# Optimization experiments

Measured on AMD Instinct MI355X. Metric: run time of the kernel, lower is better.

Reference implementation:

```python
import jax, jax.numpy as jnp
import numpy as np

B, T, D, H = 4, 1024, 512, 8
DK = D // H
P = 2 * T - 1  # relative position length


def rel_shift(x):
    # x: (b, h, t, 2t-1) -> (b, h, t, t), Transformer-XL relative shift
    b, h, t, p = x.shape
    x = jnp.pad(x, ((0, 0), (0, 0), (0, 0), (1, 0)))  # (b,h,t,p+1)
    x = x.reshape(b, h, p + 1, t)[:, :, 1:, :].reshape(b, h, t, p)
    return x[..., :t]


def setup_inputs() -> dict:
    key = jax.random.key(0)
    ks = jax.random.split(key, 16)
    s = 0.02
    return {
        "q": jax.random.normal(ks[0], (B, T, D), jnp.float32),
        "k": jax.random.normal(ks[1], (B, T, D), jnp.float32),
        "v": jax.random.normal(ks[2], (B, T, D), jnp.float32),
        "pos_emb": jax.random.normal(ks[3], (1, P, D), jnp.float32),
        "Wq": jax.random.normal(ks[4], (D, D), jnp.float32) * s,
        "bq": jnp.zeros((D,), jnp.float32),
        "Wk": jax.random.normal(ks[5], (D, D), jnp.float32) * s,
        "bk": jnp.zeros((D,), jnp.float32),
        "Wv": jax.random.normal(ks[6], (D, D), jnp.float32) * s,
        "bv": jnp.zeros((D,), jnp.float32),
        "Wp": jax.random.normal(ks[7], (D, D), jnp.float32) * s,
        "pos_bias_u": jax.random.normal(ks[8], (H, DK), jnp.float32) * s,
        "pos_bias_v": jax.random.normal(ks[9], (H, DK), jnp.float32) * s,
        "Wo": jax.random.normal(ks[10], (D, D), jnp.float32) * s,
        "bo": jnp.zeros((D,), jnp.float32),
    }


def reference(q, k, v, pos_emb, Wq, bq, Wk, bk, Wv, bv, Wp,
              pos_bias_u, pos_bias_v, Wo, bo):
    b, t, d = q.shape
    # QKV projections, split heads -> (b, t, h, dk)
    qh = (q @ Wq.T + bq).reshape(b, t, H, DK)
    kh = (k @ Wk.T + bk).reshape(b, t, H, DK)
    vh = (v @ Wv.T + bv).reshape(b, t, H, DK)
    # positional projection (no bias): (1, P, h, dk)
    ph = (pos_emb @ Wp.T).reshape(pos_emb.shape[1], H, DK)
    # content term: (q + u) . k
    q_u = qh + pos_bias_u  # (b,t,h,dk)
    matrix_ac = jnp.einsum("bqhd,bkhd->bhqk", q_u, kh)
    # position term: (q + v) . p, then relative shift
    q_v = qh + pos_bias_v
    matrix_bd = jnp.einsum("bqhd,phd->bhqp", q_v, ph)
    matrix_bd = rel_shift(matrix_bd)  # (b,h,t,t)
    scores = (matrix_ac + matrix_bd) / jnp.sqrt(jnp.float32(DK))
    attn = jax.nn.softmax(scores, axis=-1)
    out = jnp.einsum("bhqk,bkhd->bqhd", attn, vh).reshape(b, t, d)
    return out @ Wo.T + bo
```

## Files before the change

### kernel.cpp

```cpp
#include <hip/hip_runtime.h>
#include <math.h>

typedef unsigned short u16;
typedef _Float16 f16;
typedef __attribute__((ext_vector_type(8))) _Float16 f16x8;
typedef __attribute__((ext_vector_type(4))) float f32x4;

#define B_  4
#define T_  1024
#define D_  512
#define H_  8
#define DK_ 64
#define P_  2047

#define MFMAH(a, b, c) __builtin_amdgcn_mfma_f32_16x16x32_f16(a, b, c, 0, 0, 0)

__device__ __forceinline__ u16 f2hbits(float x) {
    union { f16 h; u16 u; } cv; cv.h = (f16)x; return cv.u;
}

__device__ __forceinline__ void gload_lds16(const u16* g, u16* l) {
    __builtin_amdgcn_global_load_lds(
        (const __attribute__((address_space(1))) void*)g,
        (__attribute__((address_space(3))) void*)l, 16, 0, 0);
}

__device__ __forceinline__ int swz8(int row, int colbase) {
    return row * 64 + (((colbase >> 3) ^ (row & 7)) << 3);
}

__global__ __launch_bounds__(256)
void conv_all(const float* __restrict__ q, const float* __restrict__ k,
              const float* __restrict__ v, const float* __restrict__ pe,
              const float* __restrict__ wq, const float* __restrict__ wk,
              const float* __restrict__ wv, const float* __restrict__ wp,
              const float* __restrict__ wo,
              u16* qs, u16* ks, u16* vs, u16* pes,
              u16* wqs, u16* wks, u16* wvs, u16* wps, u16* wos)
{
    const int NQ = 524288;
    const int NPE = 262016;
    const int NW = 65536;
    const int TOT = 3 * NQ + NPE + 5 * NW;
    for (int i = blockIdx.x * 256 + threadIdx.x; i < TOT; i += gridDim.x * 256) {
        const float* src; u16* dst; int off;
        int j = i;
        if (j < NQ)              { src = q;  dst = qs;  off = j; }
        else if ((j -= NQ) < NQ) { src = k;  dst = ks;  off = j; }
        else if ((j -= NQ) < NQ) { src = v;  dst = vs;  off = j; }
        else if ((j -= NQ) < NPE){ src = pe; dst = pes; off = j; }
        else if ((j -= NPE) < NW){ src = wq; dst = wqs; off = j; }
        else if ((j -= NW) < NW) { src = wk; dst = wks; off = j; }
        else if ((j -= NW) < NW) { src = wv; dst = wvs; off = j; }
        else if ((j -= NW) < NW) { src = wp; dst = wps; off = j; }
        else                     { j -= NW; src = wo; dst = wos; off = j; }
        float4 x = *(const float4*)(src + (size_t)off * 4);
        union { f16 h[4]; uint2 u2; } cv;
        cv.h[0] = (f16)x.x; cv.h[1] = (f16)x.y;
        cv.h[2] = (f16)x.z; cv.h[3] = (f16)x.w;
        *(uint2*)(dst + (size_t)off * 4) = cv.u2;
    }
}

__device__ __forceinline__ void gemm_core(
    const u16* __restrict__ A, const u16* __restrict__ Bw,
    int bm, int bn, int M, f32x4 (&acc)[4][4],
    u16 (&sA)[128][64], u16 (&sB)[128][64])
{
    const int tid = threadIdx.x;
    const int ln = tid & 63, w = tid >> 6;
    const int arow = ln & 15, kseg = ln >> 4;
    const int wr = w >> 1, wc = w & 1;

    for (int k0 = 0; k0 < 512; k0 += 64) {
        #pragma unroll
        for (int it = 0; it < 4; ++it) {
            int ch = it * 256 + tid;
            int r = ch >> 3, j = ch & 7;
            int rm = bm + r; if (rm > M - 1) rm = M - 1;
            gload_lds16(A + (size_t)rm * 512 + k0 + ((j ^ (r & 7)) << 3),
                        &sA[0][0] + ch * 8);
        }
        #pragma unroll
        for (int it = 0; it < 4; ++it) {
            int ch = it * 256 + tid;
            int r = ch >> 3, j = ch & 7;
            gload_lds16(Bw + (size_t)(bn + r) * 512 + k0 + ((j ^ (r & 7)) << 3),
                        &sB[0][0] + ch * 8);
        }
        __syncthreads();

        f16x8 af[4][2], bf[4][2];
        #pragma unroll
        for (int mi = 0; mi < 4; ++mi) {
            int row = wr * 64 + mi * 16 + arow;
            #pragma unroll
            for (int kc = 0; kc < 2; ++kc)
                af[mi][kc] = *(const f16x8*)
                    (&sA[row][0] + ((((kc << 2) | kseg) ^ (row & 7)) << 3));
        }
        #pragma unroll
        for (int nj = 0; nj < 4; ++nj) {
            int row = wc * 64 + nj * 16 + arow;
            #pragma unroll
            for (int kc = 0; kc < 2; ++kc)
                bf[nj][kc] = *(const f16x8*)
                    (&sB[row][0] + ((((kc << 2) | kseg) ^ (row & 7)) << 3));
        }
        #pragma unroll
        for (int mi = 0; mi < 4; ++mi)
            #pragma unroll
            for (int nj = 0; nj < 4; ++nj)
                #pragma unroll
                for (int kc = 0; kc < 2; ++kc)
                    acc[mi][nj] = MFMAH(af[mi][kc], bf[nj][kc], acc[mi][nj]);
        __syncthreads();
    }
}

__global__ __launch_bounds__(256, 3)
void gemm_qkvp(const u16* __restrict__ qs, const u16* __restrict__ ks,
               const u16* __restrict__ vs, const u16* __restrict__ pes,
               const u16* __restrict__ wqs, const u16* __restrict__ wks,
               const u16* __restrict__ wvs, const u16* __restrict__ wps,
               const float* __restrict__ bq, const float* __restrict__ bk,
               const float* __restrict__ bv,
               float* __restrict__ qh, u16* __restrict__ kh,
               u16* __restrict__ vt, u16* __restrict__ ph)
{
    __shared__ u16 sA[128][64];
    __shared__ u16 sB[128][64];

    const int by = blockIdx.y;
    const u16 *A, *Bw; const float* bias;
    int seg, bm, M, Tn;
    if (by < 32)      { seg=0; bm=by*128;       A=qs;  Bw=wqs; bias=bq;      M=4096; Tn=T_; }
    else if (by < 64) { seg=1; bm=(by-32)*128;  A=ks;  Bw=wks; bias=bk;      M=4096; Tn=T_; }
    else if (by < 96) { seg=2; bm=(by-64)*128;  A=vs;  Bw=wvs; bias=bv;      M=4096; Tn=T_; }
    else              { seg=3; bm=(by-96)*128;  A=pes; Bw=wps; bias=nullptr; M=P_;   Tn=P_; }
    const int bn = blockIdx.x * 128;

    f32x4 acc[4][4] = {};
    gemm_core(A, Bw, bm, bn, M, acc, sA, sB);

    const int tid = threadIdx.x;
    const int ln = tid & 63, w = tid >> 6;
    const int arow = ln & 15, kseg = ln >> 4;
    const int wr = w >> 1, wc = w & 1;

    float bv0[4];
    #pragma unroll
    for (int nj = 0; nj < 4; ++nj)
        bv0[nj] = bias ? bias[bn + wc * 64 + nj * 16 + arow] : 0.f;

    #pragma unroll
    for (int mi = 0; mi < 4; ++mi)
        #pragma unroll
        for (int r = 0; r < 4; ++r) {
            int m = bm + wr * 64 + mi * 16 + kseg * 4 + r;
            if (m >= M) continue;
            #pragma unroll
            for (int nj = 0; nj < 4; ++nj) {
                int n = bn + wc * 64 + nj * 16 + arow;
                float val = acc[mi][nj][r] + bv0[nj];
                if (seg == 0) {
                    qh[(size_t)m * 512 + n] = val;
                } else if (seg == 2) {
                    int bb = m >> 10, t = m & 1023;
                    int hh = n >> 6, d = n & 63;
                    vt[((size_t)(bb * H_ + hh) * 64 + d) * T_ + t] = f2hbits(val);
                } else {
                    int bb = (Tn == T_) ? (m >> 10) : 0;
                    int t = m - bb * Tn;
                    int hh = n >> 6, d = n & 63;
                    size_t off = ((size_t)(bb * H_ + hh) * Tn + t) * 64 + d;
                    if (seg == 1) kh[off] = f2hbits(val);
                    else          ph[off] = f2hbits(val);
                }
            }
        }
}

__global__ __launch_bounds__(256, 3)
void gemm_out(const u16* __restrict__ A, const u16* __restrict__ Bw,
              const float* __restrict__ bias, float* __restrict__ C)
{
    __shared__ u16 sA[128][64];
    __shared__ u16 sB[128][64];
    const int bn = blockIdx.x * 128;
    const int bm = blockIdx.y * 128;
    f32x4 acc[4][4] = {};
    gemm_core(A, Bw, bm, bn, 4096, acc, sA, sB);

    const int tid = threadIdx.x;
    const int ln = tid & 63, w = tid >> 6;
    const int arow = ln & 15, kseg = ln >> 4;
    const int wr = w >> 1, wc = w & 1;
    #pragma unroll
    for (int mi = 0; mi < 4; ++mi)
        #pragma unroll
        for (int r = 0; r < 4; ++r) {
            int m = bm + wr * 64 + mi * 16 + kseg * 4 + r;
            #pragma unroll
            for (int nj = 0; nj < 4; ++nj) {
                int n = bn + wc * 64 + nj * 16 + arow;
                C[(size_t)m * 512 + n] = acc[mi][nj][r] + bias[n];
            }
        }
}

__global__ __launch_bounds__(256, 2)
void relattn_mfma(const float* __restrict__ qh,
                  const u16* __restrict__ kh, const u16* __restrict__ vt,
                  const u16* __restrict__ ph,
                  const float* __restrict__ pbu, const float* __restrict__ pbv,
                  u16* __restrict__ ao)
{
    __shared__ u16 s_k[2][64][64];
    __shared__ u16 s_p[2][64][64];
    __shared__ u16 s_pp[4][16][64];

    const int tid = threadIdx.x;
    const int ln  = tid & 63;
    const int w   = tid >> 6;
    const int arow = ln & 15;
    const int kseg = ln >> 4;

    const int lg = ((blockIdx.x & 7) << 6) | (blockIdx.x >> 3);
    const int qt = lg & 15, h = (lg >> 4) & 7, b = lg >> 7;
    const int q0 = qt * 64;

    f16x8 qu[2], qv[2];
    #pragma unroll
    for (int c = 0; c < 2; ++c) {
        const float* qp = qh + ((size_t)(b * T_ + q0 + w * 16 + arow)) * D_ + h * DK_ + c * 32 + kseg * 8;
        float4 a0 = *(const float4*)qp;
        float4 a1 = *(const float4*)(qp + 4);
        const float* up = pbu + h * DK_ + c * 32 + kseg * 8;
        const float* vp = pbv + h * DK_ + c * 32 + kseg * 8;
        float4 u0 = *(const float4*)up, u1 = *(const float4*)(up + 4);
        float4 v0 = *(const float4*)vp, v1 = *(const float4*)(vp + 4);
        float qa[8] = {a0.x, a0.y, a0.z, a0.w, a1.x, a1.y, a1.z, a1.w};
        float ua[8] = {u0.x, u0.y, u0.z, u0.w, u1.x, u1.y, u1.z, u1.w};
        float va[8] = {v0.x, v0.y, v0.z, v0.w, v1.x, v1.y, v1.z, v1.w};
        #pragma unroll
        for (int i = 0; i < 8; ++i) {
            qu[c][i] = (f16)((qa[i] + ua[i]) * 0.125f);
            qv[c][i] = (f16)((qa[i] + va[i]) * 0.125f);
        }
    }

    f32x4 o_[4] = {};
    float m_run[4] = {-1e30f, -1e30f, -1e30f, -1e30f};
    float l_run[4] = {};

    const size_t kvbase = (size_t)(b * H_ + h) * T_ * 64;
    const size_t vtbase = (size_t)(b * H_ + h) * 64 * T_;
    const size_t pbase  = (size_t)h * P_ * 64;
    const int jb0 = 960 - q0;

    auto stage_k = [&](int kt, int buf) {
        #pragma unroll
        for (int it = 0; it < 2; ++it) {
            int idx = tid + it * 256;
            int r = idx >> 3, ch = idx & 7;
            const u16* src = kh + kvbase + (size_t)(kt * 64 + r) * 64 + ((ch ^ (r & 7)) << 3);
            gload_lds16(src, &s_k[buf][0][0] + idx * 8);
        }
    };
    auto stage_p = [&](int c, int slot) {
        #pragma unroll
        for (int it = 0; it < 2; ++it) {
            int idx = tid + it * 256;
            int r = idx >> 3, ch = idx & 7;
            int j = jb0 + c * 64 + r; if (j > P_ - 1) j = P_ - 1;
            const u16* src = ph + pbase + (size_t)j * 64 + ((ch ^ (r & 7)) << 3);
            gload_lds16(src, &s_p[slot][0][0] + idx * 8);
        }
    };
    auto bd_chunk = [&](int slot, f32x4* out) {
        #pragma unroll
        for (int nb = 0; nb < 4; ++nb) {
            int pr = nb * 16 + arow;
            f16x8 b0 = *(const f16x8*)(&s_p[slot][0][0] + swz8(pr, kseg * 8));
            f16x8 b1 = *(const f16x8*)(&s_p[slot][0][0] + swz8(pr, 32 + kseg * 8));
            out[nb] = MFMAH(qv[0], b0, out[nb]);
            out[nb] = MFMAH(qv[1], b1, out[nb]);
        }
    };

    stage_k(0, 0); stage_p(0, 0); stage_p(1, 1);
    __syncthreads();
    f32x4 carry[4] = {};
    bd_chunk(0, carry);
    __syncthreads();

    for (int t = 0; t < 16; ++t) {
        const int p = t & 1;
        const int k0 = t * 64;

        if (t < 15) { stage_k(t + 1, p ^ 1); stage_p(t + 2, p); }

        f16x8 vfr[4][2];
        #pragma unroll
        for (int nt = 0; nt < 4; ++nt) {
            const u16* vp = vt + vtbase + (size_t)(nt * 16 + arow) * T_ + k0 + kseg * 8;
            vfr[nt][0] = *(const f16x8*)vp;
            vfr[nt][1] = *(const f16x8*)(vp + 32);
        }

        __builtin_amdgcn_s_setprio(1);
        f32x4 ac[4] = {};
        #pragma unroll
        for (int nt = 0; nt < 4; ++nt) {
            int kr = nt * 16 + arow;
            f16x8 b0 = *(const f16x8*)(&s_k[p][0][0] + swz8(kr, kseg * 8));
            f16x8 b1 = *(const f16x8*)(&s_k[p][0][0] + swz8(kr, 32 + kseg * 8));
            ac[nt] = MFMAH(qu[0], b0, ac[nt]);
            ac[nt] = MFMAH(qu[1], b1, ac[nt]);
        }
        f32x4 bdn[4] = {};
        bd_chunk(p ^ 1, bdn);
        __builtin_amdgcn_s_setprio(0);

        float win[5][4];
        #pragma unroll
        for (int r = 0; r < 4; ++r) {
            if (w == 0)      { win[0][r]=carry[3][r]; win[1][r]=bdn[0][r];   win[2][r]=bdn[1][r];   win[3][r]=bdn[2][r];   win[4][r]=bdn[3][r]; }
            else if (w == 1) { win[0][r]=carry[2][r]; win[1][r]=carry[3][r]; win[2][r]=bdn[0][r];   win[3][r]=bdn[1][r];   win[4][r]=bdn[2][r]; }
            else if (w == 2) { win[0][r]=carry[1][r]; win[1][r]=carry[2][r]; win[2][r]=carry[3][r]; win[3][r]=bdn[0][r];   win[4][r]=bdn[1][r]; }
            else             { win[0][r]=carry[0][r]; win[1][r]=carry[1][r]; win[2][r]=carry[2][r]; win[3][r]=carry[3][r]; win[4][r]=bdn[0][r]; }
        }

        float sm[4][4];
        #pragma unroll
        for (int r = 0; r < 4; ++r) {
            int sl  = 15 - (kseg << 2) - r;
            int src = (ln & 48) | ((arow + sl) & 15);
            int cy  = (arow + sl) >> 4;
            float pm[5];
            #pragma unroll
            for (int i = 0; i < 5; ++i) pm[i] = __shfl(win[i][r], src, 64);
            #pragma unroll
            for (int nt = 0; nt < 4; ++nt)
                sm[nt][r] = ac[nt][r] + (cy ? pm[nt + 1] : pm[nt]);
        }

        #pragma unroll
        for (int r = 0; r < 4; ++r) {
            float mxv = fmaxf(fmaxf(sm[0][r], sm[1][r]), fmaxf(sm[2][r], sm[3][r]));
            #pragma unroll
            for (int off = 8; off; off >>= 1) mxv = fmaxf(mxv, __shfl_xor(mxv, off));
            float mnew = fmaxf(m_run[r], mxv);
            float fac = __expf(m_run[r] - mnew);
            m_run[r] = mnew;
            float ps = 0.f;
            int r16 = kseg * 4 + r;
            #pragma unroll
            for (int nt = 0; nt < 4; ++nt) {
                float pv = __expf(sm[nt][r] - mnew);
                ps += pv;
                int kl = nt * 16 + arow;
                s_pp[w][r16][(((kl >> 3) ^ (r16 & 7)) << 3) | (kl & 7)] = f2hbits(pv);
            }
            #pragma unroll
            for (int off = 8; off; off >>= 1) ps += __shfl_xor(ps, off);
            l_run[r] = l_run[r] * fac + ps;
            #pragma unroll
            for (int nt = 0; nt < 4; ++nt) o_[nt][r] *= fac;
        }
        asm volatile("s_waitcnt lgkmcnt(0)" ::: "memory");
        __builtin_amdgcn_sched_barrier(0);

        f16x8 pa0 = *(const f16x8*)(&s_pp[w][arow][0] + ((kseg ^ (arow & 7)) << 3));
        f16x8 pa1 = *(const f16x8*)(&s_pp[w][arow][0] + (((4 + kseg) ^ (arow & 7)) << 3));
        __builtin_amdgcn_s_setprio(1);
        #pragma unroll
        for (int nt = 0; nt < 4; ++nt) {
            o_[nt] = MFMAH(pa0, vfr[nt][0], o_[nt]);
            o_[nt] = MFMAH(pa1, vfr[nt][1], o_[nt]);
        }
        __builtin_amdgcn_s_setprio(0);

        #pragma unroll
        for (int nb = 0; nb < 4; ++nb) carry[nb] = bdn[nb];

        __syncthreads();
    }

    #pragma unroll
    for (int nt = 0; nt < 4; ++nt)
        #pragma unroll
        for (int r = 0; r < 4; ++r) {
            int qrow = q0 + w * 16 + kseg * 4 + r;
            float val = o_[nt][r] / l_run[r];
            size_t off = ((size_t)(b * T_ + qrow)) * D_ + h * DK_ + nt * 16 + arow;
            ao[off] = f2hbits(val);
        }
}

extern "C" void kernel_launch(void* const* d_in, const int* in_sizes, int n_in,
                              void* d_out, int out_size, void* d_ws, size_t ws_size,
                              hipStream_t stream)
{
    const float* q   = (const float*)d_in[0];
    const float* k   = (const float*)d_in[1];
    const float* v   = (const float*)d_in[2];
    const float* pe  = (const float*)d_in[3];
    const float* Wq  = (const float*)d_in[4];
    const float* bq  = (const float*)d_in[5];
    const float* Wk  = (const float*)d_in[6];
    const float* bk  = (const float*)d_in[7];
    const float* Wv  = (const float*)d_in[8];
    const float* bv  = (const float*)d_in[9];
    const float* Wp  = (const float*)d_in[10];
    const float* pbu = (const float*)d_in[11];
    const float* pbv = (const float*)d_in[12];
    const float* Wo  = (const float*)d_in[13];
    const float* bo  = (const float*)d_in[14];
    float* out = (float*)d_out;

    char* ws = (char*)d_ws;
    const size_t MB = 1024 * 1024;
    const size_t HMB = 512 * 1024;
    u16* qs  = (u16*)(ws);
    u16* ks  = (u16*)(ws + 4 * MB);
    u16* vs  = (u16*)(ws + 8 * MB);
    u16* pes = (u16*)(ws + 12 * MB);
    u16* wqs = (u16*)(ws + 15 * MB);
    u16* wks = (u16*)(ws + 15 * MB + HMB);
    u16* wvs = (u16*)(ws + 16 * MB);
    u16* wps = (u16*)(ws + 16 * MB + HMB);
    u16* wos = (u16*)(ws + 17 * MB);
    float* qh = (float*)(ws + 18 * MB);
    u16* kh  = (u16*)(ws + 26 * MB);
    u16* vt  = (u16*)(ws + 30 * MB);
    u16* ph  = (u16*)(ws + 34 * MB);
    u16* ao  = (u16*)(ws + 37 * MB);

    dim3 blk(256);
    conv_all<<<dim3(2048), blk, 0, stream>>>(q, k, v, pe, Wq, Wk, Wv, Wp, Wo,
        qs, ks, vs, pes, wqs, wks, wvs, wps, wos);

    gemm_qkvp<<<dim3(4, 112), blk, 0, stream>>>(
        qs, ks, vs, pes, wqs, wks, wvs, wps,
        bq, bk, bv, qh, kh, vt, ph);

    relattn_mfma<<<dim3(512), blk, 0, stream>>>(qh, kh, vt, ph, pbu, pbv, ao);

    gemm_out<<<dim3(4, 32), blk, 0, stream>>>(ao, wos, bo, out);
}
```

Baseline: 102.5 us.

## Split attention over key halves with a combine kernel; precompute f16 q+u/q+v

The relative-position attention kernel now splits the key range into two halves, so it launches twice as many blocks. Each block writes unnormalised partial outputs plus its running max and sum, and a new combine kernel merges the two halves with log-sum-exp rescaling before the output projection. Separately, the Q projection epilogue now adds the positional biases u and v, scales, and stores head-major f16 qu/qv, so the attention kernel loads those directly instead of fp32 q. This is meant to improve CU occupancy on a small grid and cut q-load bandwidth. In exchange it adds a 16 MB fp32 partial-output round trip and an extra kernel launch.

New measurement: 114.7 us. +11.9%, slower.

```diff
diff --git a/kernel.cpp b/kernel.cpp
--- a/kernel.cpp
+++ b/kernel.cpp
@@ -125,8 +125,9 @@
                const u16* __restrict__ wvs, const u16* __restrict__ wps,
                const float* __restrict__ bq, const float* __restrict__ bk,
                const float* __restrict__ bv,
-               float* __restrict__ qh, u16* __restrict__ kh,
-               u16* __restrict__ vt, u16* __restrict__ ph)
+               const float* __restrict__ pbu, const float* __restrict__ pbv,
+               u16* __restrict__ qub, u16* __restrict__ qvb,
+               u16* __restrict__ kh, u16* __restrict__ vt, u16* __restrict__ ph)
 {
     __shared__ u16 sA[128][64];
     __shared__ u16 sB[128][64];
@@ -164,7 +165,11 @@
                 int n = bn + wc * 64 + nj * 16 + arow;
                 float val = acc[mi][nj][r] + bv0[nj];
                 if (seg == 0) {
-                    qh[(size_t)m * 512 + n] = val;
+                    int bb = m >> 10, t = m & 1023;
+                    int hh = n >> 6, d = n & 63;
+                    size_t off = ((size_t)(bb * H_ + hh) * T_ + t) * 64 + d;
+                    qub[off] = f2hbits((val + pbu[hh * 64 + d]) * 0.125f);
+                    qvb[off] = f2hbits((val + pbv[hh * 64 + d]) * 0.125f);
                 } else if (seg == 2) {
                     int bb = m >> 10, t = m & 1023;
                     int hh = n >> 6, d = n & 63;
@@ -210,11 +215,10 @@
 }
 
 __global__ __launch_bounds__(256, 2)
-void relattn_mfma(const float* __restrict__ qh,
+void relattn_mfma(const u16* __restrict__ qub, const u16* __restrict__ qvb,
                   const u16* __restrict__ kh, const u16* __restrict__ vt,
                   const u16* __restrict__ ph,
-                  const float* __restrict__ pbu, const float* __restrict__ pbv,
-                  u16* __restrict__ ao)
+                  float* __restrict__ po, float2* __restrict__ pml)
 {
     __shared__ u16 s_k[2][64][64];
     __shared__ u16 s_p[2][64][64];
@@ -226,27 +230,25 @@
     const int arow = ln & 15;
     const int kseg = ln >> 4;
 
-    const int lg = ((blockIdx.x & 7) << 6) | (blockIdx.x >> 3);
-    const int qt = lg & 15, h = (lg >> 4) & 7, b = lg >> 7;
+    const int lg = ((blockIdx.x & 7) << 7) | (blockIdx.x >> 3);
+    const int qt = lg & 15, h = (lg >> 4) & 7, b = (lg >> 7) & 3;
+    const int half = lg >> 9;
     const int q0 = qt * 64;
+    const int kbase = half * 512;
+
+    const size_t kvbase = (size_t)(b * H_ + h) * T_ * 64;
+    const size_t vtbase = (size_t)(b * H_ + h) * 64 * T_;
+    const size_t pbase  = (size_t)h * P_ * 64;
+    const int jb0 = 960 - q0 + kbase;
 
     f16x8 qu[2], qv[2];
-    #pragma unroll
-    for (int c = 0; c < 2; ++c) {
-        const float* qp = qh + ((size_t)(b * T_ + q0 + w * 16 + arow)) * D_ + h * DK_ + c * 32 + kseg * 8;
-        float4 a0 = *(const float4*)qp;
-        float4 a1 = *(const float4*)(qp + 4);
-        const float* up = pbu + h * DK_ + c * 32 + kseg * 8;
-        const float* vp = pbv + h * DK_ + c * 32 + kseg * 8;
-        float4 u0 = *(const float4*)up, u1 = *(const float4*)(up + 4);
-        float4 v0 = *(const float4*)vp, v1 = *(const float4*)(vp + 4);
-        float qa[8] = {a0.x, a0.y, a0.z, a0.w, a1.x, a1.y, a1.z, a1.w};
-        float ua[8] = {u0.x, u0.y, u0.z, u0.w, u1.x, u1.y, u1.z, u1.w};
-        float va[8] = {v0.x, v0.y, v0.z, v0.w, v1.x, v1.y, v1.z, v1.w};
-        #pragma unroll
-        for (int i = 0; i < 8; ++i) {
-            qu[c][i] = (f16)((qa[i] + ua[i]) * 0.125f);
-            qv[c][i] = (f16)((qa[i] + va[i]) * 0.125f);
+    {
+        const u16* qb = qub + kvbase + (size_t)(q0 + w * 16 + arow) * 64;
+        const u16* vb = qvb + kvbase + (size_t)(q0 + w * 16 + arow) * 64;
+        #pragma unroll
+        for (int c = 0; c < 2; ++c) {
+            qu[c] = *(const f16x8*)(qb + c * 32 + kseg * 8);
+            qv[c] = *(const f16x8*)(vb + c * 32 + kseg * 8);
         }
     }
 
@@ -254,17 +256,12 @@
     float m_run[4] = {-1e30f, -1e30f, -1e30f, -1e30f};
     float l_run[4] = {};
 
-    const size_t kvbase = (size_t)(b * H_ + h) * T_ * 64;
-    const size_t vtbase = (size_t)(b * H_ + h) * 64 * T_;
-    const size_t pbase  = (size_t)h * P_ * 64;
-    const int jb0 = 960 - q0;
-
     auto stage_k = [&](int kt, int buf) {
         #pragma unroll
         for (int it = 0; it < 2; ++it) {
             int idx = tid + it * 256;
             int r = idx >> 3, ch = idx & 7;
-            const u16* src = kh + kvbase + (size_t)(kt * 64 + r) * 64 + ((ch ^ (r & 7)) << 3);
+            const u16* src = kh + kvbase + (size_t)(kbase + kt * 64 + r) * 64 + ((ch ^ (r & 7)) << 3);
             gload_lds16(src, &s_k[buf][0][0] + idx * 8);
         }
     };
@@ -295,11 +292,11 @@
     bd_chunk(0, carry);
     __syncthreads();
 
-    for (int t = 0; t < 16; ++t) {
+    for (int t = 0; t < 8; ++t) {
         const int p = t & 1;
-        const int k0 = t * 64;
-
-        if (t < 15) { stage_k(t + 1, p ^ 1); stage_p(t + 2, p); }
+        const int k0 = kbase + t * 64;
+
+        if (t < 7) { stage_k(t + 1, p ^ 1); stage_p(t + 2, p); }
 
         f16x8 vfr[4][2];
         #pragma unroll
@@ -388,15 +385,43 @@
         __syncthreads();
     }
 
+    float* poH = po + (size_t)half * 4096 * 512;
     #pragma unroll
     for (int nt = 0; nt < 4; ++nt)
         #pragma unroll
         for (int r = 0; r < 4; ++r) {
             int qrow = q0 + w * 16 + kseg * 4 + r;
-            float val = o_[nt][r] / l_run[r];
-            size_t off = ((size_t)(b * T_ + qrow)) * D_ + h * DK_ + nt * 16 + arow;
-            ao[off] = f2hbits(val);
-        }
+            poH[(size_t)(b * T_ + qrow) * 512 + h * 64 + nt * 16 + arow] = o_[nt][r];
+        }
+    if (arow == 0) {
+        #pragma unroll
+        for (int r = 0; r < 4; ++r) {
+            int qrow = q0 + w * 16 + kseg * 4 + r;
+            pml[(size_t)half * 32768 + (size_t)(b * T_ + qrow) * 8 + h] =
+                make_float2(m_run[r], l_run[r]);
+        }
+    }
+}
+
+__global__ __launch_bounds__(256)
+void combine_halves(const float4* __restrict__ po0, const float4* __restrict__ po1,
+                    const float2* __restrict__ pml0, const float2* __restrict__ pml1,
+                    u16* __restrict__ ao)
+{
+    int i = blockIdx.x * 256 + threadIdx.x;
+    int row = i >> 7;
+    int h = (i >> 4) & 7;
+    float4 o1 = po0[i], o2 = po1[i];
+    float2 a = pml0[row * 8 + h], bml = pml1[row * 8 + h];
+    float m = fmaxf(a.x, bml.x);
+    float e1 = __expf(a.x - m), e2 = __expf(bml.x - m);
+    float inv = 1.f / (a.y * e1 + bml.y * e2);
+    ushort4 r;
+    r.x = f2hbits((o1.x * e1 + o2.x * e2) * inv);
+    r.y = f2hbits((o1.y * e1 + o2.y * e2) * inv);
+    r.z = f2hbits((o1.z * e1 + o2.z * e2) * inv);
+    r.w = f2hbits((o1.w * e1 + o2.w * e2) * inv);
+    *(ushort4*)(ao + (size_t)i * 4) = r;
 }
 
 extern "C" void kernel_launch(void* const* d_in, const int* in_sizes, int n_in,
@@ -427,16 +452,19 @@
     u16* ks  = (u16*)(ws + 4 * MB);
     u16* vs  = (u16*)(ws + 8 * MB);
     u16* pes = (u16*)(ws + 12 * MB);
-    u16* wqs = (u16*)(ws + 15 * MB);
-    u16* wks = (u16*)(ws + 15 * MB + HMB);
-    u16* wvs = (u16*)(ws + 16 * MB);
-    u16* wps = (u16*)(ws + 16 * MB + HMB);
-    u16* wos = (u16*)(ws + 17 * MB);
-    float* qh = (float*)(ws + 18 * MB);
-    u16* kh  = (u16*)(ws + 26 * MB);
-    u16* vt  = (u16*)(ws + 30 * MB);
-    u16* ph  = (u16*)(ws + 34 * MB);
-    u16* ao  = (u16*)(ws + 37 * MB);
+    u16* wqs = (u16*)(ws + 17 * MB);
+    u16* wks = (u16*)(ws + 17 * MB + HMB);
+    u16* wvs = (u16*)(ws + 18 * MB);
+    u16* wps = (u16*)(ws + 18 * MB + HMB);
+    u16* wos = (u16*)(ws + 19 * MB);
+    u16* qub = (u16*)(ws + 20 * MB);
+    u16* qvb = (u16*)(ws + 24 * MB);
+    u16* kh  = (u16*)(ws + 28 * MB);
+    u16* vt  = (u16*)(ws + 32 * MB);
+    u16* ph  = (u16*)(ws + 36 * MB);
+    float*  po  = (float*)(ws);
+    float2* pml = (float2*)(ws + 16 * MB);
+    u16* ao  = (u16*)(ws + 38 * MB + HMB);
 
     dim3 blk(256);
     conv_all<<<dim3(2048), blk, 0, stream>>>(q, k, v, pe, Wq, Wk, Wv, Wp, Wo,
@@ -444,9 +472,13 @@
 
     gemm_qkvp<<<dim3(4, 112), blk, 0, stream>>>(
         qs, ks, vs, pes, wqs, wks, wvs, wps,
-        bq, bk, bv, qh, kh, vt, ph);
-
-    relattn_mfma<<<dim3(512), blk, 0, stream>>>(qh, kh, vt, ph, pbu, pbv, ao);
+        bq, bk, bv, pbu, pbv, qub, qvb, kh, vt, ph);
+
+    relattn_mfma<<<dim3(1024), blk, 0, stream>>>(qub, qvb, kh, vt, ph, po, pml);
+
+    combine_halves<<<dim3(2048), blk, 0, stream>>>(
+        (const float4*)po, (const float4*)(po + (size_t)4096 * 512),
+        pml, pml + 32768, ao);
 
     gemm_out<<<dim3(4, 32), blk, 0, stream>>>(ao, wos, bo, out);
 }
```
